# Kernel optimization log

Measured on AMD Instinct MI355X. Metric: run time of the kernel, lower is better.

The kernel has to match this reference:

```python
import jax, jax.numpy as jnp
import numpy as np

# DREAMPlace IDXST_IDCT (a.k.a. idsct2): y[u,v] = sum_p sum_q x[p,q] * sin(pi*p*(u+0.5)/M) * cos(pi*q*(v+0.5)/N)
# i.e. IDXST (inverse discrete sine transform, DST-III-like, unnormalized) along the M axis
# and IDCT (DCT-III-like, unnormalized, full weight on k=0) along the N axis.
# Computed with the classic 2N-padded FFT trick using the precomputed twiddles
# expk[k] = exp(-1j*pi*k/(2N)) stored as [N,2] (real, imag), matching precompute_expk.

def _idxt_spectrum(x, expk):
    """F[u] = sum_k x[k] * exp(-1j*pi*k*(2u+1)/(2N)), along last axis.
    Re(F) is the IDCT sum (cos), -Im(F) is the IDXST sum (sin)."""
    N = x.shape[-1]
    c = (x * expk[..., 0]) + 1j * (x * expk[..., 1])  # x[k] * exp(-j*pi*k/(2N))
    z = jnp.concatenate([c, jnp.zeros_like(c)], axis=-1)  # zero-pad to 2N
    return jnp.fft.fft(z, axis=-1)[..., :N]


def idct_1d(x, expk):
    # y[u] = sum_k x[k] cos(pi*k*(2u+1)/(2N))
    return _idxt_spectrum(x, expk).real


def idxst_1d(x, expk):
    # y[u] = sum_k x[k] sin(pi*k*(2u+1)/(2N))
    return -_idxt_spectrum(x, expk).imag


def _make_expk(L):
    k = jnp.arange(L, dtype=jnp.float32) * (np.pi / (2.0 * L))
    return jnp.stack([jnp.cos(k), -jnp.sin(k)], axis=-1)  # exp(-j*pi*k/(2L))


def setup_inputs() -> dict:
    M, N = 4096, 4096
    key = jax.random.key(0)
    x = jax.random.normal(key, (M, N), dtype=jnp.float32)
    return {"x": x, "expkM": _make_expk(M), "expkN": _make_expk(N)}


def reference(x, expkM, expkN):
    # IDCT along the last dim (N), then IDXST along the second-to-last dim (M):
    # idxst(idct(x)^T)^T
    t = idct_1d(x, expkN)                                        # [M, N]
    y = idxst_1d(t.swapaxes(-2, -1), expkM).swapaxes(-2, -1)     # [M, N]
    return y
```

## Files before the change

kernel.cpp:

```cpp
#include <hip/hip_runtime.h>
#include <hip/hip_bf16.h>
#include <stdint.h>
#include <cmath>


typedef __attribute__((ext_vector_type(4))) float f32x4;
typedef __attribute__((ext_vector_type(8))) unsigned short u16x8;
typedef __attribute__((ext_vector_type(8))) __bf16 bf16x8;

__device__ __forceinline__ unsigned short f2bf(float f) {
  union { float f; unsigned u; } v; v.f = f;
  unsigned u = v.u + 0x7fffu + ((v.u >> 16) & 1u);
  return (unsigned short)(u >> 16);
}

__device__ __forceinline__ void gen_half(int idx, u16x8* Pe, u16x8* Po,
                                         int isSin, int jshift, int jmask,
                                         unsigned mask4L, float sc) {
  int i = idx >> jshift;
  int jb = (idx & jmask) * 8;
  unsigned tp = 2u * (unsigned)i + 1u;
  unsigned re = (2u * (unsigned)jb * tp) & mask4L;
  unsigned ro = (re + tp) & mask4L;
  unsigned step = (2u * tp) & mask4L;
  u16x8 pe, po;
#pragma unroll
  for (int t = 0; t < 8; t++) {
    float se_, ce_, so_, co_;
    __sincosf((float)re * sc, &se_, &ce_);
    __sincosf((float)ro * sc, &so_, &co_);
    pe[t] = f2bf(isSin ? se_ : ce_);
    po[t] = f2bf(isSin ? so_ : co_);
    re = (re + step) & mask4L;
    ro = (ro + step) & mask4L;
  }
  Pe[idx] = pe;
  Po[idx] = po;
}

__global__ void prep_kernel(const f32x4* __restrict__ x, u16x8* __restrict__ xe,
                            u16x8* __restrict__ xo, u16x8* __restrict__ Ce,
                            u16x8* __restrict__ Co, u16x8* __restrict__ Se,
                            u16x8* __restrict__ So, int nConvBlocks,
                            int nGenNBlocks, int jshiftN, int jmaskN,
                            unsigned mask4N, float scN, int jshiftM, int jmaskM,
                            unsigned mask4M, float scM) {
  int b = blockIdx.x;
  if (b < nConvBlocks) {
    int idx = b * 256 + threadIdx.x;
    f32x4 a = x[4 * idx], bb = x[4 * idx + 1], c = x[4 * idx + 2],
          d = x[4 * idx + 3];
    u16x8 e, o;
    e[0] = f2bf(a[0]);  o[0] = f2bf(a[1]);  e[1] = f2bf(a[2]);  o[1] = f2bf(a[3]);
    e[2] = f2bf(bb[0]); o[2] = f2bf(bb[1]); e[3] = f2bf(bb[2]); o[3] = f2bf(bb[3]);
    e[4] = f2bf(c[0]);  o[4] = f2bf(c[1]);  e[5] = f2bf(c[2]);  o[5] = f2bf(c[3]);
    e[6] = f2bf(d[0]);  o[6] = f2bf(d[1]);  e[7] = f2bf(d[2]);  o[7] = f2bf(d[3]);
    xe[idx] = e;
    xo[idx] = o;
  } else if (b < nConvBlocks + nGenNBlocks) {
    int idx = (b - nConvBlocks) * 256 + threadIdx.x;
    gen_half(idx, Ce, Co, 0, jshiftN, jmaskN, mask4N, scN);
  } else {
    int idx = (b - nConvBlocks - nGenNBlocks) * 256 + threadIdx.x;
    gen_half(idx, Se, So, 1, jshiftM, jmaskM, mask4M, scM);
  }
}

#define LGKM0()                                             \
  do {                                                      \
    asm volatile("s_waitcnt lgkmcnt(0)" ::: "memory");      \
    __builtin_amdgcn_sched_barrier(0);                      \
  } while (0)
#define VMCNT6()                                            \
  do {                                                      \
    asm volatile("s_waitcnt vmcnt(6)" ::: "memory");        \
    __builtin_amdgcn_sched_barrier(0);                      \
  } while (0)
#define VMCNT0()                                            \
  do {                                                      \
    asm volatile("s_waitcnt vmcnt(0)" ::: "memory");        \
    __builtin_amdgcn_sched_barrier(0);                      \
  } while (0)
#define BAR() __builtin_amdgcn_s_barrier()

template <int STAGE>
__global__ __launch_bounds__(512, 2) void fused_gemm_kernel(
    const unsigned short* __restrict__ Ae,
    const unsigned short* __restrict__ Ao,
    const unsigned short* __restrict__ Be,
    const unsigned short* __restrict__ Bo,
    unsigned short* __restrict__ out0, unsigned short* __restrict__ out1,
    int outStride, int K, int Lfull) {
  __shared__ unsigned short AsE[128 * 64];
  __shared__ unsigned short BsE[256 * 64];
  __shared__ unsigned short AsO[128 * 64];
  __shared__ unsigned short BsO[256 * 64];

  const int tid = threadIdx.x;

  const int nwg = gridDim.x * gridDim.y;
  const int lin = blockIdx.y * gridDim.x + blockIdx.x;
  int swb = lin;
  if ((nwg & 7) == 0) swb = (lin & 7) * (nwg >> 3) + (lin >> 3);
  const int m0 = (swb / gridDim.x) * 128;
  const int n0 = (swb % gridDim.x) * 256;

  const int wave = tid >> 6;
  const int lane = tid & 63;
  const int wm = (wave >> 2) * 64;
  const int wn = (wave & 3) * 64;
  const int l16 = lane & 15;
  const int quad = lane >> 4;
  const int swz = (quad ^ (l16 & 7)) * 8;

  const int lrow = lane >> 3;
  const int lsw = ((lane & 7) ^ lrow) * 8;

  auto stage = [&](const unsigned short* __restrict__ A,
                   const unsigned short* __restrict__ B, unsigned short* As,
                   unsigned short* Bs, int k0) {
    const unsigned short* Ap =
        A + (size_t)(m0 + 8 * wave + lrow) * K + lsw + k0;
    const unsigned short* Bp =
        B + (size_t)(n0 + 8 * wave + lrow) * K + lsw + k0;
    unsigned short* Adst = As + wave * 512;
    unsigned short* Bdst = Bs + wave * 512;
#define GLL(src, dst)                                                        \
  __builtin_amdgcn_global_load_lds(                                          \
      (const __attribute__((address_space(1))) void*)(src),                  \
      (__attribute__((address_space(3))) void*)(dst), 16, 0, 0)
    GLL(Ap, Adst);
    GLL(Ap + (size_t)64 * K, Adst + 4096);
    GLL(Bp, Bdst);
    GLL(Bp + (size_t)64 * K, Bdst + 4096);
    GLL(Bp + (size_t)128 * K, Bdst + 8192);
    GLL(Bp + (size_t)192 * K, Bdst + 12288);
#undef GLL
  };

  f32x4 accE[4][4], accO[4][4];
#pragma unroll
  for (int i = 0; i < 4; i++)
#pragma unroll
    for (int j = 0; j < 4; j++) {
      accE[i][j] = f32x4{0.f, 0.f, 0.f, 0.f};
      accO[i][j] = f32x4{0.f, 0.f, 0.f, 0.f};
    }

  auto phase_h = [&](const unsigned short* As, const unsigned short* Bs,
                     int h, f32x4 (&acc)[4][4]) {
    const int so = swz ^ (h * 32);
    bf16x8 af[4], bfr[4];
#pragma unroll
    for (int i = 0; i < 4; i++)
      af[i] = *(const bf16x8*)(As + (wm + i * 16 + l16) * 64 + so);
#pragma unroll
    for (int j = 0; j < 4; j++)
      bfr[j] = *(const bf16x8*)(Bs + (wn + j * 16 + l16) * 64 + so);
    LGKM0();
    __builtin_amdgcn_s_setprio(1);
#pragma unroll
    for (int i = 0; i < 4; i++)
#pragma unroll
      for (int j = 0; j < 4; j++)
        acc[i][j] = __builtin_amdgcn_mfma_f32_16x16x32_bf16(
            af[i], bfr[j], acc[i][j], 0, 0, 0);
    __builtin_amdgcn_s_setprio(0);
  };

  stage(Ae, Be, AsE, BsE, 0);
  stage(Ao, Bo, AsO, BsO, 0);
  VMCNT6();
  BAR();

  for (int k0 = 0; k0 < K; k0 += 64) {
    const bool lastIt = (k0 + 64 >= K);

    phase_h(AsE, BsE, 0, accE);
    BAR();
    phase_h(AsE, BsE, 1, accE);
    BAR();
    if (!lastIt) {
      stage(Ae, Be, AsE, BsE, k0 + 64);
      VMCNT6();
    } else {
      VMCNT0();
    }
    BAR();

    phase_h(AsO, BsO, 0, accO);
    BAR();
    phase_h(AsO, BsO, 1, accO);
    BAR();
    if (!lastIt) {
      stage(Ao, Bo, AsO, BsO, k0 + 64);
      VMCNT6();
    } else {
      VMCNT0();
    }
    BAR();
  }

#pragma unroll
  for (int i = 0; i < 4; i++) {
#pragma unroll
    for (int j = 0; j < 4; j++) {
      int n = n0 + wn + j * 16 + l16;
      int mb = m0 + wm + i * 16 + quad * 4;
#pragma unroll
      for (int r = 0; r < 4; r++) {
        float e = accE[i][j][r];
        float o = accO[i][j][r];
        int m = mb + r;
        if (STAGE == 1) {
          unsigned short* mat = (n & 1) ? out1 : out0;
          int c = n >> 1;
          mat[(size_t)m * outStride + c] = f2bf(e + o);
          mat[(size_t)(Lfull - 1 - m) * outStride + c] = f2bf(e - o);
        } else {
          float* y = (float*)out0;
          y[(size_t)m * outStride + n] = e + o;
          y[(size_t)(Lfull - 1 - m) * outStride + n] = o - e;
        }
      }
    }
  }
}

extern "C" void kernel_launch(void* const* d_in, const int* in_sizes, int n_in,
                              void* d_out, int out_size, void* d_ws,
                              size_t ws_size, hipStream_t stream) {
  const float* x = (const float*)d_in[0];
  const int M = in_sizes[1] / 2;
  const int N = in_sizes[2] / 2;
  const size_t MN = (size_t)M * N;

  unsigned short* ws = (unsigned short*)d_ws;
  unsigned short* xe = ws;
  unsigned short* xo = ws + MN / 2;
  unsigned short* Ce = ws + MN;
  unsigned short* Co = ws + MN + MN / 4;
  unsigned short* Se = ws + MN * 3 / 2;
  unsigned short* So = ws + MN * 7 / 4;
  unsigned short* tTe = ws + MN * 2;
  unsigned short* tTo = ws + MN * 5 / 2;

  int shiftN = 0; while ((1 << shiftN) < N) shiftN++;
  int shiftM = 0; while ((1 << shiftM) < M) shiftM++;

  int nConvBlocks = (int)(MN / 16 / 256);
  int nGenNBlocks = (N / 2) * (N / 2) / 8 / 256;
  int nGenMBlocks = (M / 2) * (M / 2) / 8 / 256;
  prep_kernel<<<nConvBlocks + nGenNBlocks + nGenMBlocks, 256, 0, stream>>>(
      (const f32x4*)x, (u16x8*)xe, (u16x8*)xo, (u16x8*)Ce, (u16x8*)Co,
      (u16x8*)Se, (u16x8*)So, nConvBlocks, nGenNBlocks, shiftN - 4,
      (N / 16) - 1, (unsigned)(4 * N - 1),
      (float)(3.14159265358979323846 / (2.0 * N)), shiftM - 4, (M / 16) - 1,
      (unsigned)(4 * M - 1), (float)(3.14159265358979323846 / (2.0 * M)));

  fused_gemm_kernel<1><<<dim3(M / 256, (N / 2) / 128), 512, 0, stream>>>(
      Ce, Co, xe, xo, tTe, tTo, M / 2, N / 2, N);

  fused_gemm_kernel<2><<<dim3(N / 256, (M / 2) / 128), 512, 0, stream>>>(
      Se, So, tTe, tTo, (unsigned short*)d_out, nullptr, N, M / 2, M);
}
```

Before: 292.4 us.

## Shrink GEMM tile to 128x128 with 4 waves and restructure load pipeline

The fused GEMM kernel moves from 512-thread 128x256 tiles to 256-thread 128x128 tiles, which doubles the grid and halves the B shared-memory buffers. The odd-parity stage is now issued at the start of each iteration, before the even-parity compute, rather than afterwards. Each parity step loads both k-halves of the fragments up front and waits with a partial lgkmcnt, so MFMAs on the first half can start while the second half is still arriving. The aim is better latency hiding and fewer barriers, at the cost of less data reuse per tile and more global traffic from the smaller tiles.

Measured after the change: 266.6 us. -8.8%, faster.

```diff
diff --git a/kernel.cpp b/kernel.cpp
--- a/kernel.cpp
+++ b/kernel.cpp
@@ -66,14 +66,19 @@
   }
 }
 
+#define LGKM8()                                             \
+  do {                                                      \
+    asm volatile("s_waitcnt lgkmcnt(8)" ::: "memory");      \
+    __builtin_amdgcn_sched_barrier(0);                      \
+  } while (0)
 #define LGKM0()                                             \
   do {                                                      \
     asm volatile("s_waitcnt lgkmcnt(0)" ::: "memory");      \
     __builtin_amdgcn_sched_barrier(0);                      \
   } while (0)
-#define VMCNT6()                                            \
-  do {                                                      \
-    asm volatile("s_waitcnt vmcnt(6)" ::: "memory");        \
+#define VMCNT8()                                            \
+  do {                                                      \
+    asm volatile("s_waitcnt vmcnt(8)" ::: "memory");        \
     __builtin_amdgcn_sched_barrier(0);                      \
   } while (0)
 #define VMCNT0()                                            \
@@ -84,7 +89,7 @@
 #define BAR() __builtin_amdgcn_s_barrier()
 
 template <int STAGE>
-__global__ __launch_bounds__(512, 2) void fused_gemm_kernel(
+__global__ __launch_bounds__(256, 2) void fused_gemm_kernel(
     const unsigned short* __restrict__ Ae,
     const unsigned short* __restrict__ Ao,
     const unsigned short* __restrict__ Be,
@@ -92,9 +97,9 @@
     unsigned short* __restrict__ out0, unsigned short* __restrict__ out1,
     int outStride, int K, int Lfull) {
   __shared__ unsigned short AsE[128 * 64];
-  __shared__ unsigned short BsE[256 * 64];
+  __shared__ unsigned short BsE[128 * 64];
   __shared__ unsigned short AsO[128 * 64];
-  __shared__ unsigned short BsO[256 * 64];
+  __shared__ unsigned short BsO[128 * 64];
 
   const int tid = threadIdx.x;
 
@@ -103,12 +108,12 @@
   int swb = lin;
   if ((nwg & 7) == 0) swb = (lin & 7) * (nwg >> 3) + (lin >> 3);
   const int m0 = (swb / gridDim.x) * 128;
-  const int n0 = (swb % gridDim.x) * 256;
+  const int n0 = (swb % gridDim.x) * 128;
 
   const int wave = tid >> 6;
   const int lane = tid & 63;
-  const int wm = (wave >> 2) * 64;
-  const int wn = (wave & 3) * 64;
+  const int wm = (wave & 1) * 64;
+  const int wn = (wave >> 1) * 64;
   const int l16 = lane & 15;
   const int quad = lane >> 4;
   const int swz = (quad ^ (l16 & 7)) * 8;
@@ -116,25 +121,19 @@
   const int lrow = lane >> 3;
   const int lsw = ((lane & 7) ^ lrow) * 8;
 
-  auto stage = [&](const unsigned short* __restrict__ A,
-                   const unsigned short* __restrict__ B, unsigned short* As,
-                   unsigned short* Bs, int k0) {
-    const unsigned short* Ap =
-        A + (size_t)(m0 + 8 * wave + lrow) * K + lsw + k0;
-    const unsigned short* Bp =
-        B + (size_t)(n0 + 8 * wave + lrow) * K + lsw + k0;
-    unsigned short* Adst = As + wave * 512;
-    unsigned short* Bdst = Bs + wave * 512;
+  auto stageP = [&](const unsigned short* __restrict__ A,
+                    const unsigned short* __restrict__ B, unsigned short* As,
+                    unsigned short* Bs, int k0) {
 #define GLL(src, dst)                                                        \
   __builtin_amdgcn_global_load_lds(                                          \
       (const __attribute__((address_space(1))) void*)(src),                  \
       (__attribute__((address_space(3))) void*)(dst), 16, 0, 0)
-    GLL(Ap, Adst);
-    GLL(Ap + (size_t)64 * K, Adst + 4096);
-    GLL(Bp, Bdst);
-    GLL(Bp + (size_t)64 * K, Bdst + 4096);
-    GLL(Bp + (size_t)128 * K, Bdst + 8192);
-    GLL(Bp + (size_t)192 * K, Bdst + 12288);
+#pragma unroll
+    for (int t = 0; t < 4; t++) {
+      int ch = wave + 4 * t;
+      GLL(A + (size_t)(m0 + 8 * ch + lrow) * K + lsw + k0, As + ch * 512);
+      GLL(B + (size_t)(n0 + 8 * ch + lrow) * K + lsw + k0, Bs + ch * 512);
+    }
 #undef GLL
   };
 
@@ -147,16 +146,32 @@
       accO[i][j] = f32x4{0.f, 0.f, 0.f, 0.f};
     }
 
-  auto phase_h = [&](const unsigned short* As, const unsigned short* Bs,
-                     int h, f32x4 (&acc)[4][4]) {
-    const int so = swz ^ (h * 32);
-    bf16x8 af[4], bfr[4];
-#pragma unroll
-    for (int i = 0; i < 4; i++)
-      af[i] = *(const bf16x8*)(As + (wm + i * 16 + l16) * 64 + so);
+  auto parity = [&](const unsigned short* As, const unsigned short* Bs,
+                    f32x4 (&acc)[4][4]) {
+    const int so0 = swz;
+    const int so1 = swz ^ 32;
+    bf16x8 a0[4], b0[4], a1[4], b1[4];
+#pragma unroll
+    for (int i = 0; i < 4; i++)
+      a0[i] = *(const bf16x8*)(As + (wm + i * 16 + l16) * 64 + so0);
 #pragma unroll
     for (int j = 0; j < 4; j++)
-      bfr[j] = *(const bf16x8*)(Bs + (wn + j * 16 + l16) * 64 + so);
+      b0[j] = *(const bf16x8*)(Bs + (wn + j * 16 + l16) * 64 + so0);
+#pragma unroll
+    for (int i = 0; i < 4; i++)
+      a1[i] = *(const bf16x8*)(As + (wm + i * 16 + l16) * 64 + so1);
+#pragma unroll
+    for (int j = 0; j < 4; j++)
+      b1[j] = *(const bf16x8*)(Bs + (wn + j * 16 + l16) * 64 + so1);
+    LGKM8();
+    __builtin_amdgcn_s_setprio(1);
+#pragma unroll
+    for (int i = 0; i < 4; i++)
+#pragma unroll
+      for (int j = 0; j < 4; j++)
+        acc[i][j] = __builtin_amdgcn_mfma_f32_16x16x32_bf16(
+            a0[i], b0[j], acc[i][j], 0, 0, 0);
+    __builtin_amdgcn_s_setprio(0);
     LGKM0();
     __builtin_amdgcn_s_setprio(1);
 #pragma unroll
@@ -164,40 +179,29 @@
 #pragma unroll
       for (int j = 0; j < 4; j++)
         acc[i][j] = __builtin_amdgcn_mfma_f32_16x16x32_bf16(
-            af[i], bfr[j], acc[i][j], 0, 0, 0);
+            a1[i], b1[j], acc[i][j], 0, 0, 0);
     __builtin_amdgcn_s_setprio(0);
   };
 
-  stage(Ae, Be, AsE, BsE, 0);
-  stage(Ao, Bo, AsO, BsO, 0);
-  VMCNT6();
-  BAR();
+  stageP(Ae, Be, AsE, BsE, 0);
 
   for (int k0 = 0; k0 < K; k0 += 64) {
     const bool lastIt = (k0 + 64 >= K);
 
-    phase_h(AsE, BsE, 0, accE);
-    BAR();
-    phase_h(AsE, BsE, 1, accE);
-    BAR();
+    stageP(Ao, Bo, AsO, BsO, k0);
+    VMCNT8();
+    BAR();
+    parity(AsE, BsE, accE);
+    BAR();
+
     if (!lastIt) {
-      stage(Ae, Be, AsE, BsE, k0 + 64);
-      VMCNT6();
+      stageP(Ae, Be, AsE, BsE, k0 + 64);
+      VMCNT8();
     } else {
       VMCNT0();
     }
     BAR();
-
-    phase_h(AsO, BsO, 0, accO);
-    BAR();
-    phase_h(AsO, BsO, 1, accO);
-    BAR();
-    if (!lastIt) {
-      stage(Ao, Bo, AsO, BsO, k0 + 64);
-      VMCNT6();
-    } else {
-      VMCNT0();
-    }
+    parity(AsO, BsO, accO);
     BAR();
   }
 
@@ -258,9 +262,9 @@
       (float)(3.14159265358979323846 / (2.0 * N)), shiftM - 4, (M / 16) - 1,
       (unsigned)(4 * M - 1), (float)(3.14159265358979323846 / (2.0 * M)));
 
-  fused_gemm_kernel<1><<<dim3(M / 256, (N / 2) / 128), 512, 0, stream>>>(
+  fused_gemm_kernel<1><<<dim3(M / 128, (N / 2) / 128), 256, 0, stream>>>(
       Ce, Co, xe, xo, tTe, tTo, M / 2, N / 2, N);
 
-  fused_gemm_kernel<2><<<dim3(N / 256, (M / 2) / 128), 512, 0, stream>>>(
+  fused_gemm_kernel<2><<<dim3(N / 128, (M / 2) / 128), 256, 0, stream>>>(
       Se, So, tTe, tTo, (unsigned short*)d_out, nullptr, N, M / 2, M);
 }
```
